# Optimization experiments

Measured on AMD Instinct MI355X. Metric: run time of the kernel, lower is better.

## Reference

```python
import jax, jax.numpy as jnp
import numpy as np

F, B, L, V, E = 4, 16384, 12, 1000000, 64


def setup_inputs() -> dict:
    key = jax.random.key(0)
    k1, k2, k3, k4 = jax.random.split(key, 4)
    tables = jax.random.normal(k1, (F, V, E), dtype=jnp.float32) * 0.02
    pos_weights = jax.random.uniform(k2, (F, L), dtype=jnp.float32)  # PositionWeightedModule weights
    indices = jax.random.randint(k3, (F, B, L), 0, V, dtype=jnp.int32)
    lengths = jax.random.randint(k4, (F, B), 0, L + 1, dtype=jnp.int32)
    return {"tables": tables, "pos_weights": pos_weights, "indices": indices, "lengths": lengths}


def reference(tables, pos_weights, indices, lengths):
    # tables: [F, V, E]; pos_weights: [F, L]; indices: [F, B, L]; lengths: [F, B]
    # Position-weighted embedding bag: gather rows, scale by per-position weight,
    # sum-pool over valid positions of each jagged bag.
    mask = jnp.arange(L, dtype=lengths.dtype)[None, None, :] < lengths[:, :, None]  # [F, B, L]
    gathered = jax.vmap(lambda t, idx: t[idx])(tables, indices)  # [F, B, L, E]
    w = pos_weights[:, None, :] * mask.astype(pos_weights.dtype)  # [F, B, L]
    pooled = jnp.einsum('fble,fbl->fbe', gathered, w)  # [F, B, E]
    # concat per-feature pooled embeddings along feature dim -> [B, F*E]
    pred = jnp.transpose(pooled, (1, 0, 2)).reshape(B, F * E)
    loss = pred.mean()
    return (loss, pred)
```

## Files before the change

kernel.cpp:

```cpp
#include <hip/hip_runtime.h>

#define NF 4
#define NB 16384
#define NL 12
#define NV 1000000
#define NE 64

__global__ __launch_bounds__(256) void bag_kernel(
    const float* __restrict__ tables,
    const float* __restrict__ pos_weights,
    const int*   __restrict__ indices,
    const int*   __restrict__ lengths,
    float*       __restrict__ pred,
    float*       __restrict__ partial)
{
    const int tid  = threadIdx.x;
    const int lane = tid & 63;
    const int f    = tid >> 6;
    const int b    = blockIdx.x;

    const int len = lengths[f * NB + b];
    const int nn  = len < NL ? len : NL;

    const int*   idxp = indices + ((size_t)f * NB + b) * NL;
    const float* pw   = pos_weights + f * NL;
    const float* tbl  = tables + (size_t)f * (size_t)NV * NE;

    int   idxv[NL];
    float w[NL];
#pragma unroll
    for (int l = 0; l < NL; ++l) {
        idxv[l] = idxp[l];
        w[l]    = (l < nn) ? pw[l] : 0.0f;
    }

    float vals[NL];
#pragma unroll
    for (int l = 0; l < NL; ++l) {
        vals[l] = (l < nn) ? tbl[(size_t)idxv[l] * NE + lane] : 0.0f;
    }

    float acc = 0.0f;
#pragma unroll
    for (int l = 0; l < NL; ++l) {
        acc += w[l] * vals[l];
    }

    pred[((size_t)b * NF + f) * NE + lane] = acc;

    float s = acc;
#pragma unroll
    for (int off = 32; off > 0; off >>= 1)
        s += __shfl_down(s, off, 64);

    __shared__ float wsum[4];
    if (lane == 0) wsum[f] = s;
    __syncthreads();
    if (tid == 0)
        partial[b] = (wsum[0] + wsum[1]) + (wsum[2] + wsum[3]);
}

__global__ __launch_bounds__(256) void loss_kernel(
    const float* __restrict__ partial,
    float*       __restrict__ loss_out)
{
    const int tid  = threadIdx.x;
    const int lane = tid & 63;
    const int wv   = tid >> 6;

    float s = 0.0f;
    for (int i = tid; i < NB; i += 256)
        s += partial[i];

#pragma unroll
    for (int off = 32; off > 0; off >>= 1)
        s += __shfl_down(s, off, 64);

    __shared__ float wsum[4];
    if (lane == 0) wsum[wv] = s;
    __syncthreads();
    if (tid == 0) {
        const double denom = (double)NB * (double)NF * (double)NE;
        loss_out[0] = (float)(((double)wsum[0] + wsum[1] + wsum[2] + wsum[3]) / denom);
    }
}

extern "C" void kernel_launch(void* const* d_in, const int* in_sizes, int n_in,
                              void* d_out, int out_size, void* d_ws, size_t ws_size,
                              hipStream_t stream) {
    const float* tables      = (const float*)d_in[0];
    const float* pos_weights = (const float*)d_in[1];
    const int*   indices     = (const int*)d_in[2];
    const int*   lengths     = (const int*)d_in[3];

    float* out  = (float*)d_out;
    float* pred = out + 1;
    float* partial = (float*)d_ws;

    bag_kernel<<<NB, 256, 0, stream>>>(tables, pos_weights, indices, lengths, pred, partial);
    loss_kernel<<<1, 256, 0, stream>>>(partial, out);
}
```

Measured before the change: 1.119 ms.

## Gather embedding rows with float4 loads, four rows per wave concurrently

Each wave now splits into four 16-lane groups. Every group loads a whole 256-byte embedding row with float4 accesses, and the 12 positions are covered in 3 iterations. The bag's indices and weights are loaded once across lanes and broadcast with shuffles, and partial sums are combined with xor-shuffles before a float4 store of the output row. The aim is fewer load instructions and index reads per bag. The catch is that pred sits at a 4-byte offset from the output base, so the float4 stores are not 16-byte aligned.

```diff
diff --git a/kernel.cpp b/kernel.cpp
--- a/kernel.cpp
+++ b/kernel.cpp
@@ -22,36 +22,51 @@
     const int len = lengths[f * NB + b];
     const int nn  = len < NL ? len : NL;
 
-    const int*   idxp = indices + ((size_t)f * NB + b) * NL;
-    const float* pw   = pos_weights + f * NL;
-    const float* tbl  = tables + (size_t)f * (size_t)NV * NE;
+    const int*    idxp = indices + ((size_t)f * NB + b) * NL;
+    const float*  pw   = pos_weights + f * NL;
+    const float4* tbl  = (const float4*)(tables + (size_t)f * (size_t)NV * NE);
 
-    int   idxv[NL];
-    float w[NL];
-#pragma unroll
-    for (int l = 0; l < NL; ++l) {
-        idxv[l] = idxp[l];
-        w[l]    = (l < nn) ? pw[l] : 0.0f;
+    int   idx_l = 0;
+    float w_l   = 0.0f;
+    if (lane < NL) {
+        idx_l = idxp[lane];
+        w_l   = (lane < nn) ? pw[lane] : 0.0f;
     }
 
-    float vals[NL];
+    const int g = lane >> 4;
+    const int j = lane & 15;
+
+    float ax = 0.0f, ay = 0.0f, az = 0.0f, aw = 0.0f;
+
 #pragma unroll
-    for (int l = 0; l < NL; ++l) {
-        vals[l] = (l < nn) ? tbl[(size_t)idxv[l] * NE + lane] : 0.0f;
+    for (int i = 0; i < 3; ++i) {
+        const int l = 4 * i + g;
+        const int   my_idx = __shfl(idx_l, l, 64);
+        const float my_w   = __shfl(w_l,   l, 64);
+        if (l < nn) {
+            const float4 v = tbl[(size_t)my_idx * (NE / 4) + j];
+            ax += my_w * v.x;
+            ay += my_w * v.y;
+            az += my_w * v.z;
+            aw += my_w * v.w;
+        }
     }
 
-    float acc = 0.0f;
-#pragma unroll
-    for (int l = 0; l < NL; ++l) {
-        acc += w[l] * vals[l];
+    ax += __shfl_xor(ax, 16, 64); ax += __shfl_xor(ax, 32, 64);
+    ay += __shfl_xor(ay, 16, 64); ay += __shfl_xor(ay, 32, 64);
+    az += __shfl_xor(az, 16, 64); az += __shfl_xor(az, 32, 64);
+    aw += __shfl_xor(aw, 16, 64); aw += __shfl_xor(aw, 32, 64);
+
+    if (lane < 16) {
+        float4 outv = {ax, ay, az, aw};
+        ((float4*)pred)[((size_t)b * NF + f) * (NE / 4) + j] = outv;
     }
 
-    pred[((size_t)b * NF + f) * NE + lane] = acc;
-
-    float s = acc;
-#pragma unroll
-    for (int off = 32; off > 0; off >>= 1)
-        s += __shfl_down(s, off, 64);
+    float s = (ax + ay) + (az + aw);
+    s += __shfl_xor(s, 1, 64);
+    s += __shfl_xor(s, 2, 64);
+    s += __shfl_xor(s, 4, 64);
+    s += __shfl_xor(s, 8, 64);
 
     __shared__ float wsum[4];
     if (lane == 0) wsum[f] = s;
@@ -93,8 +108,8 @@
     const int*   indices     = (const int*)d_in[2];
     const int*   lengths     = (const int*)d_in[3];
 
-    float* out  = (float*)d_out;
-    float* pred = out + 1;
+    float* out     = (float*)d_out;
+    float* pred    = out + 1;
     float* partial = (float*)d_ws;
 
     bag_kernel<<<NB, 256, 0, stream>>>(tables, pos_weights, indices, lengths, pred, partial);
```

Measured after the change: 1.127 ms. About the same (+0.7%).
